# Optimization experiments

Hardware: AMD Instinct MI355X
Metric: run time of the kernel (lower is better)

The kernel has to match this reference:

```python
import jax, jax.numpy as jnp
import numpy as np

N_NODES = 50000
N_EDGES = 800000
LATDIM = 128
HEAD = 4


def setup_inputs() -> dict:
    key = jax.random.key(0)
    k1, k2, k3, k4, k5, k6 = jax.random.split(key, 6)
    scale = 1.0 / np.sqrt(LATDIM)  # xavier-ish scale for the square projections
    return {
        "embeds": jax.random.normal(k1, (N_NODES, LATDIM), dtype=jnp.float32),
        "qW": jax.random.normal(k2, (LATDIM, LATDIM), dtype=jnp.float32) * scale,
        "kW": jax.random.normal(k3, (LATDIM, LATDIM), dtype=jnp.float32) * scale,
        "vW": jax.random.normal(k4, (LATDIM, LATDIM), dtype=jnp.float32) * scale,
        "rows": jax.random.randint(k5, (N_EDGES,), 0, N_NODES, dtype=jnp.int32),
        "cols": jax.random.randint(k6, (N_EDGES,), 0, N_NODES, dtype=jnp.int32),
    }


def reference(embeds, qW, kW, vW, rows, cols):
    n_nodes, latdim = embeds.shape
    head_dim = latdim // HEAD
    rowEmb = embeds[rows]                         # [E, D] gather by dst
    colEmb = embeds[cols]                         # [E, D] gather by src
    q = (rowEmb @ qW).reshape(-1, HEAD, head_dim)  # [E, H, Dh]
    k = (colEmb @ kW).reshape(-1, HEAD, head_dim)
    v = (colEmb @ vW).reshape(-1, HEAD, head_dim)
    att = jnp.einsum('ehd,ehd->eh', q, k)
    att = jnp.clip(att, -10.0, 10.0)
    expAtt = jnp.exp(att)                          # [E, H]
    # segment softmax denominator via scatter-add over destination nodes
    attNorm = jax.ops.segment_sum(expAtt, rows, num_segments=n_nodes)[rows]
    att = expAtt / (attNorm + 1e-8)
    res = (att[:, :, None] * v).reshape(-1, latdim)  # [E, D]
    out = jax.ops.segment_sum(res, rows, num_segments=n_nodes)  # [N, D]
    return out
```

## Files before the change

### kernel.cpp

```cpp
#include <hip/hip_runtime.h>
#include <hip/hip_bf16.h>

#define N_NODES 50000
#define N_EDGES 800000
#define LATDIM 128
#define HEAD 4
#define SLOT_CAP 96

#define SCAT_BLOCKS ((N_EDGES / 4 + 767) / 768)
#define GEMM_BLOCKS ((N_NODES + 63) / 64)
#define LDSP 136

typedef __attribute__((ext_vector_type(8))) short short8;
typedef __attribute__((ext_vector_type(4))) float floatx4;

__device__ __forceinline__ unsigned bf16_rne_bits(float x) {
    unsigned u = __builtin_bit_cast(unsigned, x);
    return (u + 0x7fffu + ((u >> 16) & 1u)) & 0xffff0000u;
}
__device__ __forceinline__ void split_bf16(float x, short& hi, short& lo) {
    unsigned hb = bf16_rne_bits(x);
    hi = (short)(hb >> 16);
    float hf = __builtin_bit_cast(float, hb);
    unsigned lb = bf16_rne_bits(x - hf);
    lo = (short)(lb >> 16);
}

__global__ __launch_bounds__(768) void mega_kernel(
    const float* __restrict__ E,
    const float* __restrict__ qW, const float* __restrict__ kW,
    const float* __restrict__ vW,
    const int* __restrict__ rows, const int* __restrict__ cols,
    int* __restrict__ cnt, int* __restrict__ slots,
    float* __restrict__ Q, unsigned short* __restrict__ KV2)
{
    __shared__ short AhL[64 * LDSP];
    __shared__ short AlL[64 * LDSP];

    if (blockIdx.x < SCAT_BLOCKS) {
        const int t = blockIdx.x * 768 + threadIdx.x;
        if (t < N_EDGES / 4) {
            int4 r = ((const int4*)rows)[t];
            int4 c = ((const int4*)cols)[t];
            int p;
            p = atomicAdd(&cnt[r.x], 1);
            if (p < SLOT_CAP) slots[(size_t)r.x * SLOT_CAP + p] = c.x;
            p = atomicAdd(&cnt[r.y], 1);
            if (p < SLOT_CAP) slots[(size_t)r.y * SLOT_CAP + p] = c.y;
            p = atomicAdd(&cnt[r.z], 1);
            if (p < SLOT_CAP) slots[(size_t)r.z * SLOT_CAP + p] = c.z;
            p = atomicAdd(&cnt[r.w], 1);
            if (p < SLOT_CAP) slots[(size_t)r.w * SLOT_CAP + p] = c.w;
        }
        return;
    }

    const int r_base = (blockIdx.x - SCAT_BLOCKS) * 64;

    for (int chnk = threadIdx.x; chnk < 2048; chnk += 768) {
        const int row = chnk >> 5, c4 = chnk & 31;
        int grow = r_base + row;
        if (grow > N_NODES - 1) grow = N_NODES - 1;
        float4 x = ((const float4*)E)[(size_t)grow * 32 + c4];
        short h0, l0, h1, l1, h2, l2, h3, l3;
        split_bf16(x.x, h0, l0);
        split_bf16(x.y, h1, l1);
        split_bf16(x.z, h2, l2);
        split_bf16(x.w, h3, l3);
        *(short4*)(AhL + row * LDSP + c4 * 4) = make_short4(h0, h1, h2, h3);
        *(short4*)(AlL + row * LDSP + c4 * 4) = make_short4(l0, l1, l2, l3);
    }

    const int wave = threadIdx.x >> 6;
    const int lane = threadIdx.x & 63;
    const int which = wave >> 2;
    const int n_base = (wave & 3) * 32;
    const int ln = lane & 15;
    const int q  = lane >> 4;

    const float* Wsrc = (which == 0) ? qW : (which == 1) ? kW : vW;
    short8 Bh[2][4], Bl[2][4];
#pragma unroll
    for (int tIdx = 0; tIdx < 2; ++tIdx)
#pragma unroll
        for (int c = 0; c < 4; ++c) {
            short hv[8], lv[8];
#pragma unroll
            for (int j = 0; j < 8; ++j) {
                float w = Wsrc[(c * 32 + q * 8 + j) * 128 + n_base + tIdx * 16 + ln];
                split_bf16(w, hv[j], lv[j]);
            }
            Bh[tIdx][c] = *(short8*)hv;
            Bl[tIdx][c] = *(short8*)lv;
        }

    __syncthreads();

    const int vs = (which == 2) ? 32 : 0;
    const int c0 = n_base + ln;
    const int c1 = n_base + 16 + ln;

    for (int rt = 0; rt < 4; ++rt) {
        const short* ah = AhL + (rt * 16 + ln) * LDSP + q * 8;
        const short* al = AlL + (rt * 16 + ln) * LDSP + q * 8;

        floatx4 acc0 = {0.f, 0.f, 0.f, 0.f};
        floatx4 acc1 = {0.f, 0.f, 0.f, 0.f};
#pragma unroll
        for (int c = 0; c < 4; ++c) {
            short8 Ah = *(const short8*)(ah + c * 32);
            short8 Al = *(const short8*)(al + c * 32);
            acc0 = __builtin_amdgcn_mfma_f32_16x16x32_bf16(Ah, Bh[0][c], acc0, 0, 0, 0);
            acc0 = __builtin_amdgcn_mfma_f32_16x16x32_bf16(Ah, Bl[0][c], acc0, 0, 0, 0);
            acc0 = __builtin_amdgcn_mfma_f32_16x16x32_bf16(Al, Bh[0][c], acc0, 0, 0, 0);
            acc1 = __builtin_amdgcn_mfma_f32_16x16x32_bf16(Ah, Bh[1][c], acc1, 0, 0, 0);
            acc1 = __builtin_amdgcn_mfma_f32_16x16x32_bf16(Ah, Bl[1][c], acc1, 0, 0, 0);
            acc1 = __builtin_amdgcn_mfma_f32_16x16x32_bf16(Al, Bh[1][c], acc1, 0, 0, 0);
        }

        const int r0 = r_base + rt * 16;
#pragma unroll
        for (int r = 0; r < 4; ++r) {
            const int row = r0 + q * 4 + r;
            if (row >= N_NODES) continue;
            if (which == 0) {
                Q[(size_t)row * 128 + c0] = acc0[r];
                Q[(size_t)row * 128 + c1] = acc1[r];
            } else {
                KV2[(size_t)row * 256 + (c0 >> 5) * 64 + (c0 & 31) + vs] =
                    (unsigned short)(bf16_rne_bits(acc0[r]) >> 16);
                KV2[(size_t)row * 256 + (c1 >> 5) * 64 + (c1 & 31) + vs] =
                    (unsigned short)(bf16_rne_bits(acc1[r]) >> 16);
            }
        }
    }
}

__global__ __launch_bounds__(256) void fused_kernel(
    const float* __restrict__ Q,
    const unsigned short* __restrict__ KV2,
    const int* __restrict__ cnt,
    const int* __restrict__ slots,
    float* __restrict__ out)
{
    const int n = blockIdx.x * 4 + (threadIdx.x >> 6);
    if (n >= N_NODES) return;
    const int lane = threadIdx.x & 63;
    const int s  = lane & 1;
    const int h  = (lane >> 1) & 3;
    const int el = lane >> 3;

    int deg = cnt[n];
    if (deg > SLOT_CAP) deg = SLOT_CAP;

    float qv[16];
    {
        const float4* qp = (const float4*)(Q + (size_t)n * 128 + h * 32 + s * 16);
#pragma unroll
        for (int j = 0; j < 4; ++j) {
            float4 t = qp[j];
            qv[4 * j + 0] = t.x; qv[4 * j + 1] = t.y;
            qv[4 * j + 2] = t.z; qv[4 * j + 3] = t.w;
        }
    }

    float acc[16];
#pragma unroll
    for (int j = 0; j < 16; ++j) acc[j] = 0.f;
    float norm = 0.f;

    const int* srow = slots + (size_t)n * SLOT_CAP;

    for (int i = 0; i < deg; i += 8) {
        const int e = i + el;
        if (e < deg) {
            const int col = srow[e];
            const unsigned short* kp = KV2 + (size_t)col * 256 + h * 64 + s * 16;
            uint4 k0 = *(const uint4*)(kp);
            uint4 k1 = *(const uint4*)(kp + 8);
            uint4 v0 = *(const uint4*)(kp + 32);
            uint4 v1 = *(const uint4*)(kp + 40);

            unsigned kw[8] = {k0.x, k0.y, k0.z, k0.w, k1.x, k1.y, k1.z, k1.w};
            float p = 0.f;
#pragma unroll
            for (int d = 0; d < 8; ++d) {
                float flo = __builtin_bit_cast(float, kw[d] << 16);
                float fhi = __builtin_bit_cast(float, kw[d] & 0xffff0000u);
                p += qv[2 * d] * flo + qv[2 * d + 1] * fhi;
            }
            p += __shfl_xor(p, 1);

            float a = expf(fminf(fmaxf(p, -10.0f), 10.0f));
            norm += a;

            unsigned vw[8] = {v0.x, v0.y, v0.z, v0.w, v1.x, v1.y, v1.z, v1.w};
#pragma unroll
            for (int d = 0; d < 8; ++d) {
                float flo = __builtin_bit_cast(float, vw[d] << 16);
                float fhi = __builtin_bit_cast(float, vw[d] & 0xffff0000u);
                acc[2 * d]     += a * flo;
                acc[2 * d + 1] += a * fhi;
            }
        }
    }

#pragma unroll
    for (int m = 8; m <= 32; m <<= 1) {
        norm += __shfl_xor(norm, m, 64);
#pragma unroll
        for (int j = 0; j < 16; ++j) acc[j] += __shfl_xor(acc[j], m, 64);
    }

    if (el == 0) {
        const float inv = 1.0f / (norm + 1e-8f);
        float4* op = (float4*)(out + (size_t)n * 128 + h * 32 + s * 16);
#pragma unroll
        for (int j = 0; j < 4; ++j)
            op[j] = make_float4(acc[4 * j] * inv, acc[4 * j + 1] * inv,
                                acc[4 * j + 2] * inv, acc[4 * j + 3] * inv);
    }
}

extern "C" void kernel_launch(void* const* d_in, const int* in_sizes, int n_in,
                              void* d_out, int out_size, void* d_ws, size_t ws_size,
                              hipStream_t stream) {
    const float* embeds = (const float*)d_in[0];
    const float* qW     = (const float*)d_in[1];
    const float* kW     = (const float*)d_in[2];
    const float* vW     = (const float*)d_in[3];
    const int*   rows   = (const int*)d_in[4];
    const int*   cols   = (const int*)d_in[5];
    float* out = (float*)d_out;

    float* Q = (float*)d_ws;
    unsigned short* KV2 = (unsigned short*)(Q + (size_t)N_NODES * LATDIM);
    int* cnt   = (int*)(KV2 + (size_t)N_NODES * 256);
    int* slots = cnt + N_NODES;

    hipMemsetAsync(cnt, 0, sizeof(int) * N_NODES, stream);

    mega_kernel<<<SCAT_BLOCKS + GEMM_BLOCKS, 768, 0, stream>>>(
        embeds, qW, kW, vW, rows, cols, cnt, slots, Q, KV2);

    fused_kernel<<<(N_NODES + 3) / 4, 256, 0, stream>>>(
        Q, KV2, cnt, slots, out);
}
```

Baseline: 212.0 us.

## Merge memset, scatter/GEMM and attention into one cooperative persistent kernel

Replaces the memset plus two launches with a single cooperative kernel that zeroes counts, runs the edge scatter and projection GEMM tiles in a persistent loop, then does the per-node attention after grid-wide syncs. Slot storage shrinks to 16-bit column indices with a smaller slot cap, and the GEMM block is reduced to 512 threads with waves looping over K and V. The aim is to remove launch overhead and shrink the slot traffic. In exchange, grid syncs serialise the phases, the persistent grid may under-occupy the gather phase, and the lower cap could drop edges on high-degree nodes.

```diff
diff --git a/kernel.cpp b/kernel.cpp
--- a/kernel.cpp
+++ b/kernel.cpp
@@ -1,15 +1,20 @@
 #include <hip/hip_runtime.h>
 #include <hip/hip_bf16.h>
+#include <hip/hip_cooperative_groups.h>
+
+namespace cg = cooperative_groups;
 
 #define N_NODES 50000
 #define N_EDGES 800000
 #define LATDIM 128
-#define HEAD 4
-#define SLOT_CAP 96
-
-#define SCAT_BLOCKS ((N_EDGES / 4 + 767) / 768)
-#define GEMM_BLOCKS ((N_NODES + 63) / 64)
+#define SLOT_CAP 64
 #define LDSP 136
+#define TPB 512
+#define MAX_BLOCKS 512
+
+#define SCAT_UNITS ((N_EDGES / 4 + TPB - 1) / TPB)
+#define GEMM_TILES ((N_NODES + 63) / 64)
+#define TOTAL_UNITS (SCAT_UNITS + GEMM_TILES)
 
 typedef __attribute__((ext_vector_type(8))) short short8;
 typedef __attribute__((ext_vector_type(4))) float floatx4;
@@ -26,126 +31,126 @@
     lo = (short)(lb >> 16);
 }
 
-__global__ __launch_bounds__(768) void mega_kernel(
+__device__ __forceinline__ void dev_scatter(
+    int u, int tid, const int* __restrict__ rows, const int* __restrict__ cols,
+    int* __restrict__ cnt, unsigned short* __restrict__ slots)
+{
+    const int t = u * TPB + tid;
+    if (t < N_EDGES / 4) {
+        int4 r = ((const int4*)rows)[t];
+        int4 c = ((const int4*)cols)[t];
+        int p;
+        p = atomicAdd(&cnt[r.x], 1);
+        if (p < SLOT_CAP) slots[(size_t)r.x * SLOT_CAP + p] = (unsigned short)c.x;
+        p = atomicAdd(&cnt[r.y], 1);
+        if (p < SLOT_CAP) slots[(size_t)r.y * SLOT_CAP + p] = (unsigned short)c.y;
+        p = atomicAdd(&cnt[r.z], 1);
+        if (p < SLOT_CAP) slots[(size_t)r.z * SLOT_CAP + p] = (unsigned short)c.z;
+        p = atomicAdd(&cnt[r.w], 1);
+        if (p < SLOT_CAP) slots[(size_t)r.w * SLOT_CAP + p] = (unsigned short)c.w;
+    }
+}
+
+__device__ __forceinline__ void dev_gemm_tile(
+    int tile, int tid,
     const float* __restrict__ E,
     const float* __restrict__ qW, const float* __restrict__ kW,
     const float* __restrict__ vW,
-    const int* __restrict__ rows, const int* __restrict__ cols,
-    int* __restrict__ cnt, int* __restrict__ slots,
-    float* __restrict__ Q, unsigned short* __restrict__ KV2)
-{
-    __shared__ short AhL[64 * LDSP];
-    __shared__ short AlL[64 * LDSP];
-
-    if (blockIdx.x < SCAT_BLOCKS) {
-        const int t = blockIdx.x * 768 + threadIdx.x;
-        if (t < N_EDGES / 4) {
-            int4 r = ((const int4*)rows)[t];
-            int4 c = ((const int4*)cols)[t];
-            int p;
-            p = atomicAdd(&cnt[r.x], 1);
-            if (p < SLOT_CAP) slots[(size_t)r.x * SLOT_CAP + p] = c.x;
-            p = atomicAdd(&cnt[r.y], 1);
-            if (p < SLOT_CAP) slots[(size_t)r.y * SLOT_CAP + p] = c.y;
-            p = atomicAdd(&cnt[r.z], 1);
-            if (p < SLOT_CAP) slots[(size_t)r.z * SLOT_CAP + p] = c.z;
-            p = atomicAdd(&cnt[r.w], 1);
-            if (p < SLOT_CAP) slots[(size_t)r.w * SLOT_CAP + p] = c.w;
-        }
-        return;
-    }
-
-    const int r_base = (blockIdx.x - SCAT_BLOCKS) * 64;
-
-    for (int chnk = threadIdx.x; chnk < 2048; chnk += 768) {
-        const int row = chnk >> 5, c4 = chnk & 31;
+    float* __restrict__ Q, unsigned short* __restrict__ KV2,
+    short* AhL, short* AlL)
+{
+    const int r_base = tile * 64;
+
+    __syncthreads();
+    for (int chnk = tid; chnk < 1024; chnk += TPB) {
+        const int row = chnk >> 4, c8 = chnk & 15;
         int grow = r_base + row;
         if (grow > N_NODES - 1) grow = N_NODES - 1;
-        float4 x = ((const float4*)E)[(size_t)grow * 32 + c4];
-        short h0, l0, h1, l1, h2, l2, h3, l3;
-        split_bf16(x.x, h0, l0);
-        split_bf16(x.y, h1, l1);
-        split_bf16(x.z, h2, l2);
-        split_bf16(x.w, h3, l3);
-        *(short4*)(AhL + row * LDSP + c4 * 4) = make_short4(h0, h1, h2, h3);
-        *(short4*)(AlL + row * LDSP + c4 * 4) = make_short4(l0, l1, l2, l3);
-    }
-
-    const int wave = threadIdx.x >> 6;
-    const int lane = threadIdx.x & 63;
-    const int which = wave >> 2;
-    const int n_base = (wave & 3) * 32;
+        float4 xa = ((const float4*)E)[(size_t)grow * 32 + c8 * 2 + 0];
+        float4 xb = ((const float4*)E)[(size_t)grow * 32 + c8 * 2 + 1];
+        float x[8] = {xa.x, xa.y, xa.z, xa.w, xb.x, xb.y, xb.z, xb.w};
+        short hv[8], lv[8];
+#pragma unroll
+        for (int i = 0; i < 8; ++i) split_bf16(x[i], hv[i], lv[i]);
+        *(short8*)(AhL + row * LDSP + c8 * 8) = *(short8*)hv;
+        *(short8*)(AlL + row * LDSP + c8 * 8) = *(short8*)lv;
+    }
+    __syncthreads();
+
+    const int wave = tid >> 6;
+    const int lane = tid & 63;
     const int ln = lane & 15;
     const int q  = lane >> 4;
-
-    const float* Wsrc = (which == 0) ? qW : (which == 1) ? kW : vW;
-    short8 Bh[2][4], Bl[2][4];
-#pragma unroll
-    for (int tIdx = 0; tIdx < 2; ++tIdx)
-#pragma unroll
-        for (int c = 0; c < 4; ++c) {
-            short hv[8], lv[8];
-#pragma unroll
-            for (int j = 0; j < 8; ++j) {
-                float w = Wsrc[(c * 32 + q * 8 + j) * 128 + n_base + tIdx * 16 + ln];
-                split_bf16(w, hv[j], lv[j]);
-            }
-            Bh[tIdx][c] = *(short8*)hv;
-            Bl[tIdx][c] = *(short8*)lv;
+    const int n_base = (wave & 3) * 32;
+    const int grp = wave >> 2;
+    const int wBeg = grp ? 1 : 0;
+    const int wEnd = grp ? 2 : 0;
+
+    for (int which = wBeg; which <= wEnd; ++which) {
+        const float* Wsrc = (which == 0) ? qW : (which == 1) ? kW : vW;
+        short8 Bh[2][4], Bl[2][4];
+#pragma unroll
+        for (int tIdx = 0; tIdx < 2; ++tIdx)
+#pragma unroll
+            for (int c = 0; c < 4; ++c) {
+                short hv[8], lv[8];
+#pragma unroll
+                for (int j = 0; j < 8; ++j) {
+                    float w = Wsrc[(c * 32 + q * 8 + j) * 128 +
+                                   n_base + tIdx * 16 + ln];
+                    split_bf16(w, hv[j], lv[j]);
+                }
+                Bh[tIdx][c] = *(short8*)hv;
+                Bl[tIdx][c] = *(short8*)lv;
+            }
+
+        const int vs = (which == 2) ? 32 : 0;
+        const int c0 = n_base + ln;
+        const int c1 = n_base + 16 + ln;
+
+        for (int rt = 0; rt < 4; ++rt) {
+            const short* ah = AhL + (rt * 16 + ln) * LDSP + q * 8;
+            const short* al = AlL + (rt * 16 + ln) * LDSP + q * 8;
+
+            floatx4 acc0 = {0.f, 0.f, 0.f, 0.f};
+            floatx4 acc1 = {0.f, 0.f, 0.f, 0.f};
+#pragma unroll
+            for (int c = 0; c < 4; ++c) {
+                short8 Ah = *(const short8*)(ah + c * 32);
+                short8 Al = *(const short8*)(al + c * 32);
+                acc0 = __builtin_amdgcn_mfma_f32_16x16x32_bf16(Ah, Bh[0][c], acc0, 0, 0, 0);
+                acc0 = __builtin_amdgcn_mfma_f32_16x16x32_bf16(Ah, Bl[0][c], acc0, 0, 0, 0);
+                acc0 = __builtin_amdgcn_mfma_f32_16x16x32_bf16(Al, Bh[0][c], acc0, 0, 0, 0);
+                acc1 = __builtin_amdgcn_mfma_f32_16x16x32_bf16(Ah, Bh[1][c], acc1, 0, 0, 0);
+                acc1 = __builtin_amdgcn_mfma_f32_16x16x32_bf16(Ah, Bl[1][c], acc1, 0, 0, 0);
+                acc1 = __builtin_amdgcn_mfma_f32_16x16x32_bf16(Al, Bh[1][c], acc1, 0, 0, 0);
+            }
+
+            const int r0 = r_base + rt * 16;
+#pragma unroll
+            for (int r = 0; r < 4; ++r) {
+                const int row = r0 + q * 4 + r;
+                if (row >= N_NODES) continue;
+                if (which == 0) {
+                    Q[(size_t)row * 128 + c0] = acc0[r];
+                    Q[(size_t)row * 128 + c1] = acc1[r];
+                } else {
+                    KV2[(size_t)row * 256 + (c0 >> 5) * 64 + (c0 & 31) + vs] =
+                        (unsigned short)(bf16_rne_bits(acc0[r]) >> 16);
+                    KV2[(size_t)row * 256 + (c1 >> 5) * 64 + (c1 & 31) + vs] =
+                        (unsigned short)(bf16_rne_bits(acc1[r]) >> 16);
+                }
+            }
         }
-
-    __syncthreads();
-
-    const int vs = (which == 2) ? 32 : 0;
-    const int c0 = n_base + ln;
-    const int c1 = n_base + 16 + ln;
-
-    for (int rt = 0; rt < 4; ++rt) {
-        const short* ah = AhL + (rt * 16 + ln) * LDSP + q * 8;
-        const short* al = AlL + (rt * 16 + ln) * LDSP + q * 8;
-
-        floatx4 acc0 = {0.f, 0.f, 0.f, 0.f};
-        floatx4 acc1 = {0.f, 0.f, 0.f, 0.f};
-#pragma unroll
-        for (int c = 0; c < 4; ++c) {
-            short8 Ah = *(const short8*)(ah + c * 32);
-            short8 Al = *(const short8*)(al + c * 32);
-            acc0 = __builtin_amdgcn_mfma_f32_16x16x32_bf16(Ah, Bh[0][c], acc0, 0, 0, 0);
-            acc0 = __builtin_amdgcn_mfma_f32_16x16x32_bf16(Ah, Bl[0][c], acc0, 0, 0, 0);
-            acc0 = __builtin_amdgcn_mfma_f32_16x16x32_bf16(Al, Bh[0][c], acc0, 0, 0, 0);
-            acc1 = __builtin_amdgcn_mfma_f32_16x16x32_bf16(Ah, Bh[1][c], acc1, 0, 0, 0);
-            acc1 = __builtin_amdgcn_mfma_f32_16x16x32_bf16(Ah, Bl[1][c], acc1, 0, 0, 0);
-            acc1 = __builtin_amdgcn_mfma_f32_16x16x32_bf16(Al, Bh[1][c], acc1, 0, 0, 0);
-        }
-
-        const int r0 = r_base + rt * 16;
-#pragma unroll
-        for (int r = 0; r < 4; ++r) {
-            const int row = r0 + q * 4 + r;
-            if (row >= N_NODES) continue;
-            if (which == 0) {
-                Q[(size_t)row * 128 + c0] = acc0[r];
-                Q[(size_t)row * 128 + c1] = acc1[r];
-            } else {
-                KV2[(size_t)row * 256 + (c0 >> 5) * 64 + (c0 & 31) + vs] =
-                    (unsigned short)(bf16_rne_bits(acc0[r]) >> 16);
-                KV2[(size_t)row * 256 + (c1 >> 5) * 64 + (c1 & 31) + vs] =
-                    (unsigned short)(bf16_rne_bits(acc1[r]) >> 16);
-            }
-        }
-    }
-}
-
-__global__ __launch_bounds__(256) void fused_kernel(
-    const float* __restrict__ Q,
-    const unsigned short* __restrict__ KV2,
-    const int* __restrict__ cnt,
-    const int* __restrict__ slots,
+    }
+}
+
+__device__ __forceinline__ void dev_fused(
+    int n, int lane,
+    const float* __restrict__ Q, const unsigned short* __restrict__ KV2,
+    const int* __restrict__ cnt, const unsigned short* __restrict__ slots,
     float* __restrict__ out)
 {
-    const int n = blockIdx.x * 4 + (threadIdx.x >> 6);
-    if (n >= N_NODES) return;
-    const int lane = threadIdx.x & 63;
     const int s  = lane & 1;
     const int h  = (lane >> 1) & 3;
     const int el = lane >> 3;
@@ -169,12 +174,12 @@
     for (int j = 0; j < 16; ++j) acc[j] = 0.f;
     float norm = 0.f;
 
-    const int* srow = slots + (size_t)n * SLOT_CAP;
+    const unsigned short* srow = slots + (size_t)n * SLOT_CAP;
 
     for (int i = 0; i < deg; i += 8) {
         const int e = i + el;
         if (e < deg) {
-            const int col = srow[e];
+            const int col = (int)srow[e];
             const unsigned short* kp = KV2 + (size_t)col * 256 + h * 64 + s * 16;
             uint4 k0 = *(const uint4*)(kp);
             uint4 k1 = *(const uint4*)(kp + 8);
@@ -220,6 +225,68 @@
             op[j] = make_float4(acc[4 * j] * inv, acc[4 * j + 1] * inv,
                                 acc[4 * j + 2] * inv, acc[4 * j + 3] * inv);
     }
+}
+
+__global__ __launch_bounds__(TPB, 4) void coop_kernel(
+    const float* __restrict__ E,
+    const float* __restrict__ qW, const float* __restrict__ kW,
+    const float* __restrict__ vW,
+    const int* __restrict__ rows, const int* __restrict__ cols,
+    int* __restrict__ cnt, unsigned short* __restrict__ slots,
+    float* __restrict__ Q, unsigned short* __restrict__ KV2,
+    float* __restrict__ out)
+{
+    __shared__ short AhL[64 * LDSP];
+    __shared__ short AlL[64 * LDSP];
+
+    cg::grid_group grid = cg::this_grid();
+    const int tid = threadIdx.x;
+    const int nb  = gridDim.x;
+
+    for (int i = blockIdx.x * TPB + tid; i < N_NODES; i += nb * TPB)
+        cnt[i] = 0;
+    __threadfence();
+    grid.sync();
+
+    for (int u = blockIdx.x; u < TOTAL_UNITS; u += nb) {
+        if (u < SCAT_UNITS)
+            dev_scatter(u, tid, rows, cols, cnt, slots);
+        else
+            dev_gemm_tile(u - SCAT_UNITS, tid, E, qW, kW, vW, Q, KV2, AhL, AlL);
+    }
+    __threadfence();
+    grid.sync();
+
+    const int wpb = TPB / 64;
+    for (int n = blockIdx.x * wpb + (tid >> 6); n < N_NODES; n += nb * wpb)
+        dev_fused(n, tid & 63, Q, KV2, cnt, slots, out);
+}
+
+__global__ __launch_bounds__(TPB) void phase1_kernel(
+    const float* __restrict__ E,
+    const float* __restrict__ qW, const float* __restrict__ kW,
+    const float* __restrict__ vW,
+    const int* __restrict__ rows, const int* __restrict__ cols,
+    int* __restrict__ cnt, unsigned short* __restrict__ slots,
+    float* __restrict__ Q, unsigned short* __restrict__ KV2)
+{
+    __shared__ short AhL[64 * LDSP];
+    __shared__ short AlL[64 * LDSP];
+    const int u = blockIdx.x;
+    if (u < SCAT_UNITS)
+        dev_scatter(u, threadIdx.x, rows, cols, cnt, slots);
+    else
+        dev_gemm_tile(u - SCAT_UNITS, threadIdx.x, E, qW, kW, vW, Q, KV2, AhL, AlL);
+}
+
+__global__ __launch_bounds__(256) void fused_kernel(
+    const float* __restrict__ Q, const unsigned short* __restrict__ KV2,
+    const int* __restrict__ cnt, const unsigned short* __restrict__ slots,
+    float* __restrict__ out)
+{
+    const int n = blockIdx.x * 4 + (threadIdx.x >> 6);
+    if (n < N_NODES)
+        dev_fused(n, threadIdx.x & 63, Q, KV2, cnt, slots, out);
 }
 
 extern "C" void kernel_launch(void* const* d_in, const int* in_sizes, int n_in,
@@ -235,14 +302,30 @@
 
     float* Q = (float*)d_ws;
     unsigned short* KV2 = (unsigned short*)(Q + (size_t)N_NODES * LATDIM);
-    int* cnt   = (int*)(KV2 + (size_t)N_NODES * 256);
-    int* slots = cnt + N_NODES;
-
-    hipMemsetAsync(cnt, 0, sizeof(int) * N_NODES, stream);
-
-    mega_kernel<<<SCAT_BLOCKS + GEMM_BLOCKS, 768, 0, stream>>>(
-        embeds, qW, kW, vW, rows, cols, cnt, slots, Q, KV2);
-
-    fused_kernel<<<(N_NODES + 3) / 4, 256, 0, stream>>>(
-        Q, KV2, cnt, slots, out);
-}
+    int* cnt = (int*)(KV2 + (size_t)N_NODES * 256);
+    unsigned short* slots = (unsigned short*)(cnt + N_NODES);
+
+    int occ = 0;
+    hipError_t qerr = hipOccupancyMaxActiveBlocksPerMultiprocessor(
+        &occ, (const void*)coop_kernel, TPB, 0);
+    int nblk = (qerr == hipSuccess && occ > 0) ? occ * 256 : 0;
+    if (nblk > MAX_BLOCKS) nblk = MAX_BLOCKS;
+
+    bool coop_ok = (nblk >= 1);
+    if (coop_ok) {
+        void* args[] = {(void*)&embeds, (void*)&qW, (void*)&kW, (void*)&vW,
+                        (void*)&rows, (void*)&cols, (void*)&cnt, (void*)&slots,
+                        (void*)&Q, (void*)&KV2, (void*)&out};
+        hipError_t err = hipLaunchCooperativeKernel(
+            (const void*)coop_kernel, dim3(nblk), dim3(TPB), args, 0, stream);
+        if (err != hipSuccess) coop_ok = false;
+    }
+
+    if (!coop_ok) {
+        hipMemsetAsync(cnt, 0, sizeof(int) * N_NODES, stream);
+        phase1_kernel<<<TOTAL_UNITS, TPB, 0, stream>>>(
+            embeds, qW, kW, vW, rows, cols, cnt, slots, Q, KV2);
+        fused_kernel<<<(N_NODES + 3) / 4, 256, 0, stream>>>(
+            Q, KV2, cnt, slots, out);
+    }
+}
```

Result: slower. 681.7 us (+221.5%).
